# Optimization experiments

Hardware: AMD Instinct MI355X
Metric: run time of the kernel (lower is better)

The kernel has to match this reference:

```python
import jax, jax.numpy as jnp
import numpy as np
from jax import lax

B, C, H, W = 32, 3, 128, 128
NUM_CLASSES = 101
H2, W2 = H // 2, W // 2
N = H2 * W2                      # 4096 graph nodes


def _grid_graph(h, w):
    """4-neighbor bidirectional grid graph + self loops, with GCN sym-norm coeffs."""
    idx = np.arange(h * w).reshape(h, w)
    src = np.concatenate([idx[:, :-1].ravel(), idx[:, 1:].ravel(),
                          idx[:-1, :].ravel(), idx[1:, :].ravel()])
    dst = np.concatenate([idx[:, 1:].ravel(), idx[:, :-1].ravel(),
                          idx[1:, :].ravel(), idx[:-1, :].ravel()])
    # GCNConv default: add self loops, then D^{-1/2} (A+I) D^{-1/2}
    loop = np.arange(h * w)
    src = np.concatenate([src, loop])
    dst = np.concatenate([dst, loop])
    deg = np.bincount(dst, minlength=h * w).astype(np.float32)
    dinv = 1.0 / np.sqrt(deg)
    norm = dinv[src] * dinv[dst]
    return src.astype(np.int32), dst.astype(np.int32), norm.astype(np.float32)


def setup_inputs() -> dict:
    key = jax.random.key(0)
    ks = jax.random.split(key, 9)
    x = jax.random.normal(ks[0], (B, C, H, W), dtype=jnp.float32)
    conv_w = jax.random.normal(ks[1], (32, C, 3, 3), dtype=jnp.float32) * 0.1
    conv_b = jax.random.normal(ks[2], (32,), dtype=jnp.float32) * 0.01
    gcn_w = jax.random.normal(ks[3], (32, 64), dtype=jnp.float32) * 0.15
    gcn_b = jax.random.normal(ks[4], (64,), dtype=jnp.float32) * 0.01
    fc1_w = jax.random.normal(ks[5], (128, 64 * N), dtype=jnp.float32) * (1.0 / 512.0)
    fc1_b = jax.random.normal(ks[6], (128,), dtype=jnp.float32) * 0.01
    fc2_w = jax.random.normal(ks[7], (NUM_CLASSES, 128), dtype=jnp.float32) * 0.08
    fc2_b = jax.random.normal(ks[8], (NUM_CLASSES,), dtype=jnp.float32) * 0.01
    return {"x": x, "conv_w": conv_w, "conv_b": conv_b, "gcn_w": gcn_w,
            "gcn_b": gcn_b, "fc1_w": fc1_w, "fc1_b": fc1_b,
            "fc2_w": fc2_w, "fc2_b": fc2_b}


def reference(x, conv_w, conv_b, gcn_w, gcn_b, fc1_w, fc1_b, fc2_w, fc2_b):
    # conv1 (3x3, pad=1) + relu + maxpool 2x2
    y = lax.conv_general_dilated(x, conv_w, (1, 1), "SAME",
                                 dimension_numbers=("NCHW", "OIHW", "NCHW"))
    y = jax.nn.relu(y + conv_b[None, :, None, None])
    y = lax.reduce_window(y, -jnp.inf, lax.max, (1, 1, 2, 2), (1, 1, 2, 2), "VALID")
    b, c, h2, w2 = y.shape  # [B, 32, 64, 64]

    # faithful torch x.view(B, -1, 32): raw row-major reinterpretation (NOT transpose)
    xg = y.reshape(b, -1, c)  # [B, N, 32]

    # GCNConv(32 -> 64): linear, then gather -> normalize -> scatter-add
    hfeat = jnp.einsum("bnf,fo->bno", xg, gcn_w)  # [B, N, 64]
    src, dst, norm = _grid_graph(h2, w2)
    src = jnp.asarray(src); dst = jnp.asarray(dst)
    coeff = jnp.asarray(norm, hfeat.dtype)[None, :, None]
    msgs = hfeat[:, src, :] * coeff                      # edge-wise gather
    agg = jnp.zeros_like(hfeat).at[:, dst, :].add(msgs)  # scatter-add
    g = jax.nn.relu(agg + gcn_b)

    # flatten + FCs
    flat = g.reshape(b, -1)  # [B, 64*N]
    f1 = jax.nn.relu(flat @ fc1_w.T + fc1_b)
    return f1 @ fc2_w.T + fc2_b
```

## Files before the change

kernel.cpp:

```cpp
#include <hip/hip_runtime.h>


#define K_FC 262144

__global__ __launch_bounds__(256) void k_conv_pool(
    const float* __restrict__ x, const float* __restrict__ cw,
    const float* __restrict__ cb, float* __restrict__ y)
{
    __shared__ float wl[864];
    __shared__ float tin[3 * 34 * 36];

    int blk = blockIdx.x;
    int b = blk >> 4;
    int tile = blk & 15;
    int ph0 = (tile >> 2) << 4;
    int pw0 = (tile & 3) << 4;
    int t = threadIdx.x;

    for (int i = t; i < 864; i += 256) wl[i] = cw[i];

    int r0 = ph0 * 2 - 1;
    int c0 = pw0 * 2 - 1;
    for (int i = t; i < 3 * 34 * 34; i += 256) {
        int ci = i / 1156;
        int rem = i - ci * 1156;
        int yy = rem / 34;
        int xx = rem - yy * 34;
        int gr = r0 + yy, gc = c0 + xx;
        float v = 0.f;
        if (gr >= 0 && gr < 128 && gc >= 0 && gc < 128)
            v = x[((b * 3 + ci) * 128 + gr) * 128 + gc];
        tin[ci * 1224 + yy * 36 + xx] = v;
    }
    __syncthreads();

    int ph = t >> 4, pw = t & 15;
    float p[3][4][4];
#pragma unroll
    for (int ci = 0; ci < 3; ++ci)
#pragma unroll
        for (int dy = 0; dy < 4; ++dy) {
            const float2* row = (const float2*)&tin[ci * 1224 + (2 * ph + dy) * 36 + 2 * pw];
            float2 v0 = row[0], v1 = row[1];
            p[ci][dy][0] = v0.x; p[ci][dy][1] = v0.y;
            p[ci][dy][2] = v1.x; p[ci][dy][3] = v1.y;
        }

    int obase = (b * 32 * 64 + (ph0 + ph)) * 64 + pw0 + pw;
    for (int co = 0; co < 32; ++co) {
        float s00 = 0.f, s01 = 0.f, s10 = 0.f, s11 = 0.f;
#pragma unroll
        for (int ci = 0; ci < 3; ++ci)
#pragma unroll
            for (int ky = 0; ky < 3; ++ky)
#pragma unroll
                for (int kx = 0; kx < 3; ++kx) {
                    float wv = wl[co * 27 + ci * 9 + ky * 3 + kx];
                    s00 = fmaf(p[ci][ky][kx],         wv, s00);
                    s01 = fmaf(p[ci][ky][kx + 1],     wv, s01);
                    s10 = fmaf(p[ci][ky + 1][kx],     wv, s10);
                    s11 = fmaf(p[ci][ky + 1][kx + 1], wv, s11);
                }
        float m = fmaxf(fmaxf(s00, s01), fmaxf(s10, s11)) + cb[co];
        y[obase + co * 4096] = fmaxf(m, 0.f);
    }
}

__device__ __forceinline__ float dinvf(int h, int w) {
    int d = 1 + (w > 0) + (w < 63) + (h > 0) + (h < 63);
    return rsqrtf((float)d);
}

__device__ __forceinline__ void acc4(const float* __restrict__ yb, int hq, int wq,
                                     int fh, float c,
                                     float4& a0, float4& a1, float4& a2, float4& a3)
{
    const float4* s = (const float4*)(yb + (((hq << 6) + wq) << 5) + fh);
    float4 v0 = s[0], v1 = s[1], v2 = s[2], v3 = s[3];
    a0.x = fmaf(c, v0.x, a0.x); a0.y = fmaf(c, v0.y, a0.y);
    a0.z = fmaf(c, v0.z, a0.z); a0.w = fmaf(c, v0.w, a0.w);
    a1.x = fmaf(c, v1.x, a1.x); a1.y = fmaf(c, v1.y, a1.y);
    a1.z = fmaf(c, v1.z, a1.z); a1.w = fmaf(c, v1.w, a1.w);
    a2.x = fmaf(c, v2.x, a2.x); a2.y = fmaf(c, v2.y, a2.y);
    a2.z = fmaf(c, v2.z, a2.z); a2.w = fmaf(c, v2.w, a2.w);
    a3.x = fmaf(c, v3.x, a3.x); a3.y = fmaf(c, v3.y, a3.y);
    a3.z = fmaf(c, v3.z, a3.z); a3.w = fmaf(c, v3.w, a3.w);
}

__global__ __launch_bounds__(256) void k_gcn(
    const float* __restrict__ y, const float* __restrict__ gw,
    const float* __restrict__ gb, float* __restrict__ g)
{
    __shared__ float zl[128 * 36];

    int blk = blockIdx.x;
    int b = blk >> 5;
    int r = blk & 31;
    int t = threadIdx.x;
    const float* yb = y + b * 131072;

    int lane = t & 63;
    int wave = t >> 6;
    float wreg[32];
#pragma unroll
    for (int f = 0; f < 32; ++f) wreg[f] = gw[f * 64 + lane];
    float bias = gb[lane];

    {
        int l = t >> 1;
        int fh = (t & 1) << 4;
        int h = 2 * r + (l >> 6);
        int w = l & 63;
        float dp = dinvf(h, w);
        float4 a0 = {0,0,0,0}, a1 = {0,0,0,0}, a2 = {0,0,0,0}, a3 = {0,0,0,0};
        acc4(yb, h, w, fh, dp * dp, a0, a1, a2, a3);
        if (w > 0)  acc4(yb, h, w - 1, fh, dp * dinvf(h, w - 1), a0, a1, a2, a3);
        if (w < 63) acc4(yb, h, w + 1, fh, dp * dinvf(h, w + 1), a0, a1, a2, a3);
        if (h > 0)  acc4(yb, h - 1, w, fh, dp * dinvf(h - 1, w), a0, a1, a2, a3);
        if (h < 63) acc4(yb, h + 1, w, fh, dp * dinvf(h + 1, w), a0, a1, a2, a3);
        float4* zrow = (float4*)&zl[l * 36 + fh];
        zrow[0] = a0; zrow[1] = a1; zrow[2] = a2; zrow[3] = a3;
    }
    __syncthreads();

    int l0 = wave << 5;
    int pbase = r * 128;
    float* gout = g + (size_t)b * 262144;
    for (int n = 0; n < 32; ++n) {
        int l = l0 + n;
        const float4* zz = (const float4*)&zl[l * 36];
        float acc = bias;
#pragma unroll
        for (int f4 = 0; f4 < 8; ++f4) {
            float4 zv = zz[f4];
            acc = fmaf(zv.x, wreg[f4 * 4 + 0], acc);
            acc = fmaf(zv.y, wreg[f4 * 4 + 1], acc);
            acc = fmaf(zv.z, wreg[f4 * 4 + 2], acc);
            acc = fmaf(zv.w, wreg[f4 * 4 + 3], acc);
        }
        gout[(pbase + l) * 64 + lane] = fmaxf(acc, 0.f);
    }
}

__global__ __launch_bounds__(256, 4) void k_fc1(
    const float* __restrict__ flat, const float* __restrict__ w,
    float* __restrict__ partial)
{
    __shared__ float Wl[128 * 36];
    __shared__ float Al[32 * 36];

    int t = threadIdx.x;
    int blk = blockIdx.x;
    int k0 = blk << 8;

    int sub = t >> 7;
    int tt = t & 127;
    int bg = tt >> 4;
    int b0 = bg << 2;
    int jg = tt & 15;

    float acc[4][8];
#pragma unroll
    for (int i = 0; i < 4; ++i)
#pragma unroll
        for (int jj = 0; jj < 8; ++jj) acc[i][jj] = 0.f;

    for (int s = 0; s < 8; ++s) {
        int ks = k0 + (s << 5);
#pragma unroll
        for (int it = 0; it < 4; ++it) {
            int i = t + (it << 8);
            int j = i >> 3, kq = i & 7;
            float4 v = *(const float4*)(w + (size_t)j * K_FC + ks + (kq << 2));
            *(float4*)&Wl[j * 36 + (kq << 2)] = v;
        }
        {
            int b = t >> 3, kq = t & 7;
            float4 v = *(const float4*)(flat + (size_t)b * K_FC + ks + (kq << 2));
            *(float4*)&Al[b * 36 + (kq << 2)] = v;
        }
        __syncthreads();

#pragma unroll
        for (int c = 0; c < 4; ++c) {
            int kk = (sub << 4) + (c << 2);
            float4 av[4];
#pragma unroll
            for (int i = 0; i < 4; ++i)
                av[i] = *(const float4*)&Al[(b0 + i) * 36 + kk];
#pragma unroll
            for (int jj = 0; jj < 8; ++jj) {
                float4 wv = *(const float4*)&Wl[(jg + (jj << 4)) * 36 + kk];
#pragma unroll
                for (int i = 0; i < 4; ++i) {
                    acc[i][jj] = fmaf(av[i].x, wv.x, acc[i][jj]);
                    acc[i][jj] = fmaf(av[i].y, wv.y, acc[i][jj]);
                    acc[i][jj] = fmaf(av[i].z, wv.z, acc[i][jj]);
                    acc[i][jj] = fmaf(av[i].w, wv.w, acc[i][jj]);
                }
            }
        }
        __syncthreads();
    }

    if (sub == 1) {
#pragma unroll
        for (int i = 0; i < 4; ++i)
#pragma unroll
            for (int jj = 0; jj < 8; ++jj)
                Wl[((i << 3) + jj) * 128 + tt] = acc[i][jj];
    }
    __syncthreads();
    if (sub == 0) {
        float* pout = partial + ((size_t)blk << 12);
#pragma unroll
        for (int i = 0; i < 4; ++i)
#pragma unroll
            for (int jj = 0; jj < 8; ++jj)
                pout[(b0 + i) * 128 + jg + (jj << 4)] =
                    acc[i][jj] + Wl[((i << 3) + jj) * 128 + tt];
    }
}

__global__ __launch_bounds__(256) void k_red(
    const float* __restrict__ partial, float* __restrict__ f1)
{
    __shared__ float4 Sl[256];
    int t = threadIdx.x;
    int e4 = (blockIdx.x << 2) + (t & 3);
    int ng = t >> 2;
    const float4* p = (const float4*)partial;
    float4 a = {0.f, 0.f, 0.f, 0.f};
#pragma unroll
    for (int i = 0; i < 16; ++i) {
        int ns = ng + (i << 6);
        float4 v = p[(size_t)ns * 1024 + e4];
        a.x += v.x; a.y += v.y; a.z += v.z; a.w += v.w;
    }
    Sl[t] = a;
    __syncthreads();
    for (int off = 128; off >= 4; off >>= 1) {
        if (t < off) {
            float4 u = Sl[t], v = Sl[t + off];
            u.x += v.x; u.y += v.y; u.z += v.z; u.w += v.w;
            Sl[t] = u;
        }
        __syncthreads();
    }
    if (t < 4) ((float4*)f1)[(blockIdx.x << 2) + t] = Sl[t];
}

__global__ __launch_bounds__(256) void k_fc2(
    const float* __restrict__ f1, const float* __restrict__ b1,
    const float* __restrict__ w2, const float* __restrict__ b2,
    float* __restrict__ out)
{
    int idx = blockIdx.x * 256 + threadIdx.x;
    if (idx >= 32 * 101) return;
    int b = idx / 101;
    int c = idx - b * 101;
    const float4* fp = (const float4*)(f1 + b * 128);
    const float4* bp = (const float4*)b1;
    const float4* wp = (const float4*)(w2 + c * 128);
    float acc = b2[c];
#pragma unroll
    for (int q = 0; q < 32; ++q) {
        float4 f = fp[q], bb = bp[q], ww = wp[q];
        acc = fmaf(fmaxf(f.x + bb.x, 0.f), ww.x, acc);
        acc = fmaf(fmaxf(f.y + bb.y, 0.f), ww.y, acc);
        acc = fmaf(fmaxf(f.z + bb.z, 0.f), ww.z, acc);
        acc = fmaf(fmaxf(f.w + bb.w, 0.f), ww.w, acc);
    }
    out[idx] = acc;
}

extern "C" void kernel_launch(void* const* d_in, const int* in_sizes, int n_in,
                              void* d_out, int out_size, void* d_ws, size_t ws_size,
                              hipStream_t stream)
{
    const float* x  = (const float*)d_in[0];
    const float* cw = (const float*)d_in[1];
    const float* cb = (const float*)d_in[2];
    const float* gw = (const float*)d_in[3];
    const float* gb = (const float*)d_in[4];
    const float* w1 = (const float*)d_in[5];
    const float* b1 = (const float*)d_in[6];
    const float* w2 = (const float*)d_in[7];
    const float* b2 = (const float*)d_in[8];
    float* out = (float*)d_out;

    float* y       = (float*)d_ws;
    float* g       = y + 4194304;
    float* partial = g + 8388608;
    float* f1      = partial + 4194304;

    k_conv_pool<<<512, 256, 0, stream>>>(x, cw, cb, y);
    k_gcn<<<1024, 256, 0, stream>>>(y, gw, gb, g);
    k_fc1<<<1024, 256, 0, stream>>>(g, w1, partial);
    k_red<<<256, 256, 0, stream>>>(partial, f1);
    k_fc2<<<13, 256, 0, stream>>>(f1, b1, w2, b2, out);
}
```

Before: 281.3 us.

## Restructure GCN linear as register-tiled GEMM and stream fc1 weights directly

The GCN transform now stages aggregated features transposed in shared memory along with the weights and bias, and computes a 4x8 register tile per thread instead of a per-lane dot loop with 32 weight registers. The fc1 split-K kernel stops staging weight tiles in shared memory. It loads the whole 256-wide activation slab once, then each thread streams float4 weight chunks for two output rows straight from global memory, accumulates all 32 batch rows, and reduces across a 4-lane group with shuffles. This targets the fc1 weight traffic, which dominates runtime, by cutting the per-step syncs and LDS round trips. In exchange it uses 64 accumulators per thread, lowering occupancy (launch bounds changed to 3 blocks per CU).

```diff
diff --git a/kernel.cpp b/kernel.cpp
--- a/kernel.cpp
+++ b/kernel.cpp
@@ -91,7 +91,9 @@
     const float* __restrict__ y, const float* __restrict__ gw,
     const float* __restrict__ gb, float* __restrict__ g)
 {
-    __shared__ float zl[128 * 36];
+    __shared__ float zl[32 * 132];
+    __shared__ float wl[32 * 64];
+    __shared__ float bl[64];
 
     int blk = blockIdx.x;
     int b = blk >> 5;
@@ -99,126 +101,138 @@
     int t = threadIdx.x;
     const float* yb = y + b * 131072;
 
-    int lane = t & 63;
-    int wave = t >> 6;
-    float wreg[32];
-#pragma unroll
-    for (int f = 0; f < 32; ++f) wreg[f] = gw[f * 64 + lane];
-    float bias = gb[lane];
+    for (int i = t; i < 512; i += 256) ((float4*)wl)[i] = ((const float4*)gw)[i];
+    if (t < 64) bl[t] = gb[t];
 
     {
         int l = t >> 1;
         int fh = (t & 1) << 4;
         int h = 2 * r + (l >> 6);
-        int w = l & 63;
-        float dp = dinvf(h, w);
+        int wq = l & 63;
+        float dp = dinvf(h, wq);
         float4 a0 = {0,0,0,0}, a1 = {0,0,0,0}, a2 = {0,0,0,0}, a3 = {0,0,0,0};
-        acc4(yb, h, w, fh, dp * dp, a0, a1, a2, a3);
-        if (w > 0)  acc4(yb, h, w - 1, fh, dp * dinvf(h, w - 1), a0, a1, a2, a3);
-        if (w < 63) acc4(yb, h, w + 1, fh, dp * dinvf(h, w + 1), a0, a1, a2, a3);
-        if (h > 0)  acc4(yb, h - 1, w, fh, dp * dinvf(h - 1, w), a0, a1, a2, a3);
-        if (h < 63) acc4(yb, h + 1, w, fh, dp * dinvf(h + 1, w), a0, a1, a2, a3);
-        float4* zrow = (float4*)&zl[l * 36 + fh];
-        zrow[0] = a0; zrow[1] = a1; zrow[2] = a2; zrow[3] = a3;
+        acc4(yb, h, wq, fh, dp * dp, a0, a1, a2, a3);
+        if (wq > 0)  acc4(yb, h, wq - 1, fh, dp * dinvf(h, wq - 1), a0, a1, a2, a3);
+        if (wq < 63) acc4(yb, h, wq + 1, fh, dp * dinvf(h, wq + 1), a0, a1, a2, a3);
+        if (h > 0)   acc4(yb, h - 1, wq, fh, dp * dinvf(h - 1, wq), a0, a1, a2, a3);
+        if (h < 63)  acc4(yb, h + 1, wq, fh, dp * dinvf(h + 1, wq), a0, a1, a2, a3);
+        zl[(fh + 0)  * 132 + l] = a0.x; zl[(fh + 1)  * 132 + l] = a0.y;
+        zl[(fh + 2)  * 132 + l] = a0.z; zl[(fh + 3)  * 132 + l] = a0.w;
+        zl[(fh + 4)  * 132 + l] = a1.x; zl[(fh + 5)  * 132 + l] = a1.y;
+        zl[(fh + 6)  * 132 + l] = a1.z; zl[(fh + 7)  * 132 + l] = a1.w;
+        zl[(fh + 8)  * 132 + l] = a2.x; zl[(fh + 9)  * 132 + l] = a2.y;
+        zl[(fh + 10) * 132 + l] = a2.z; zl[(fh + 11) * 132 + l] = a2.w;
+        zl[(fh + 12) * 132 + l] = a3.x; zl[(fh + 13) * 132 + l] = a3.y;
+        zl[(fh + 14) * 132 + l] = a3.z; zl[(fh + 15) * 132 + l] = a3.w;
     }
     __syncthreads();
 
-    int l0 = wave << 5;
+    int fg = t & 7;
+    int ng = t >> 3;
+    int n0 = ng << 2;
+    int f0 = fg << 3;
+
+    float acc[4][8];
+#pragma unroll
+    for (int i = 0; i < 4; ++i)
+#pragma unroll
+        for (int jj = 0; jj < 8; ++jj) acc[i][jj] = 0.f;
+
+#pragma unroll 8
+    for (int k = 0; k < 32; ++k) {
+        float4 zv  = *(const float4*)&zl[k * 132 + n0];
+        float4 wv0 = *(const float4*)&wl[(k << 6) + f0];
+        float4 wv1 = *(const float4*)&wl[(k << 6) + f0 + 4];
+        float zs[4] = {zv.x, zv.y, zv.z, zv.w};
+        float ws[8] = {wv0.x, wv0.y, wv0.z, wv0.w, wv1.x, wv1.y, wv1.z, wv1.w};
+#pragma unroll
+        for (int i = 0; i < 4; ++i)
+#pragma unroll
+            for (int jj = 0; jj < 8; ++jj)
+                acc[i][jj] = fmaf(zs[i], ws[jj], acc[i][jj]);
+    }
+
     int pbase = r * 128;
     float* gout = g + (size_t)b * 262144;
-    for (int n = 0; n < 32; ++n) {
-        int l = l0 + n;
-        const float4* zz = (const float4*)&zl[l * 36];
-        float acc = bias;
-#pragma unroll
-        for (int f4 = 0; f4 < 8; ++f4) {
-            float4 zv = zz[f4];
-            acc = fmaf(zv.x, wreg[f4 * 4 + 0], acc);
-            acc = fmaf(zv.y, wreg[f4 * 4 + 1], acc);
-            acc = fmaf(zv.z, wreg[f4 * 4 + 2], acc);
-            acc = fmaf(zv.w, wreg[f4 * 4 + 3], acc);
-        }
-        gout[(pbase + l) * 64 + lane] = fmaxf(acc, 0.f);
-    }
-}
-
-__global__ __launch_bounds__(256, 4) void k_fc1(
+#pragma unroll
+    for (int i = 0; i < 4; ++i) {
+        float4 o0, o1;
+        o0.x = fmaxf(acc[i][0] + bl[f0 + 0], 0.f);
+        o0.y = fmaxf(acc[i][1] + bl[f0 + 1], 0.f);
+        o0.z = fmaxf(acc[i][2] + bl[f0 + 2], 0.f);
+        o0.w = fmaxf(acc[i][3] + bl[f0 + 3], 0.f);
+        o1.x = fmaxf(acc[i][4] + bl[f0 + 4], 0.f);
+        o1.y = fmaxf(acc[i][5] + bl[f0 + 5], 0.f);
+        o1.z = fmaxf(acc[i][6] + bl[f0 + 6], 0.f);
+        o1.w = fmaxf(acc[i][7] + bl[f0 + 7], 0.f);
+        float* op = gout + (size_t)(pbase + n0 + i) * 64 + f0;
+        *(float4*)op = o0;
+        *(float4*)(op + 4) = o1;
+    }
+}
+
+__global__ __launch_bounds__(256, 3) void k_fc1(
     const float* __restrict__ flat, const float* __restrict__ w,
     float* __restrict__ partial)
 {
-    __shared__ float Wl[128 * 36];
-    __shared__ float Al[32 * 36];
+    __shared__ float Al[32 * 264];
 
     int t = threadIdx.x;
     int blk = blockIdx.x;
     int k0 = blk << 8;
 
-    int sub = t >> 7;
-    int tt = t & 127;
-    int bg = tt >> 4;
-    int b0 = bg << 2;
-    int jg = tt & 15;
-
-    float acc[4][8];
-#pragma unroll
-    for (int i = 0; i < 4; ++i)
-#pragma unroll
-        for (int jj = 0; jj < 8; ++jj) acc[i][jj] = 0.f;
-
-    for (int s = 0; s < 8; ++s) {
-        int ks = k0 + (s << 5);
-#pragma unroll
-        for (int it = 0; it < 4; ++it) {
-            int i = t + (it << 8);
-            int j = i >> 3, kq = i & 7;
-            float4 v = *(const float4*)(w + (size_t)j * K_FC + ks + (kq << 2));
-            *(float4*)&Wl[j * 36 + (kq << 2)] = v;
+#pragma unroll
+    for (int rr = 0; rr < 8; ++rr) {
+        int idx = (rr << 8) + t;
+        int b = idx >> 6;
+        int c4 = (idx & 63) << 2;
+        *(float4*)&Al[b * 264 + c4] =
+            *(const float4*)(flat + (size_t)b * K_FC + k0 + c4);
+    }
+    __syncthreads();
+
+    int s = t & 3;
+    int j2 = t >> 2;
+    const float* wr0 = w + (size_t)j2 * K_FC + k0 + (s << 2);
+    const float* wr1 = wr0 + (size_t)64 * K_FC;
+
+    float acc0[32], acc1[32];
+#pragma unroll
+    for (int b = 0; b < 32; ++b) { acc0[b] = 0.f; acc1[b] = 0.f; }
+
+#pragma unroll 2
+    for (int q = 0; q < 16; ++q) {
+        float4 wa = *(const float4*)(wr0 + (q << 4));
+        float4 wb = *(const float4*)(wr1 + (q << 4));
+        int kk = (q << 4) + (s << 2);
+#pragma unroll
+        for (int b = 0; b < 32; ++b) {
+            float4 a = *(const float4*)&Al[b * 264 + kk];
+            acc0[b] = fmaf(a.x, wa.x, acc0[b]);
+            acc0[b] = fmaf(a.y, wa.y, acc0[b]);
+            acc0[b] = fmaf(a.z, wa.z, acc0[b]);
+            acc0[b] = fmaf(a.w, wa.w, acc0[b]);
+            acc1[b] = fmaf(a.x, wb.x, acc1[b]);
+            acc1[b] = fmaf(a.y, wb.y, acc1[b]);
+            acc1[b] = fmaf(a.z, wb.z, acc1[b]);
+            acc1[b] = fmaf(a.w, wb.w, acc1[b]);
         }
-        {
-            int b = t >> 3, kq = t & 7;
-            float4 v = *(const float4*)(flat + (size_t)b * K_FC + ks + (kq << 2));
-            *(float4*)&Al[b * 36 + (kq << 2)] = v;
-        }
-        __syncthreads();
-
-#pragma unroll
-        for (int c = 0; c < 4; ++c) {
-            int kk = (sub << 4) + (c << 2);
-            float4 av[4];
-#pragma unroll
-            for (int i = 0; i < 4; ++i)
-                av[i] = *(const float4*)&Al[(b0 + i) * 36 + kk];
-#pragma unroll
-            for (int jj = 0; jj < 8; ++jj) {
-                float4 wv = *(const float4*)&Wl[(jg + (jj << 4)) * 36 + kk];
-#pragma unroll
-                for (int i = 0; i < 4; ++i) {
-                    acc[i][jj] = fmaf(av[i].x, wv.x, acc[i][jj]);
-                    acc[i][jj] = fmaf(av[i].y, wv.y, acc[i][jj]);
-                    acc[i][jj] = fmaf(av[i].z, wv.z, acc[i][jj]);
-                    acc[i][jj] = fmaf(av[i].w, wv.w, acc[i][jj]);
-                }
-            }
-        }
-        __syncthreads();
-    }
-
-    if (sub == 1) {
-#pragma unroll
-        for (int i = 0; i < 4; ++i)
-#pragma unroll
-            for (int jj = 0; jj < 8; ++jj)
-                Wl[((i << 3) + jj) * 128 + tt] = acc[i][jj];
-    }
-    __syncthreads();
-    if (sub == 0) {
-        float* pout = partial + ((size_t)blk << 12);
-#pragma unroll
-        for (int i = 0; i < 4; ++i)
-#pragma unroll
-            for (int jj = 0; jj < 8; ++jj)
-                pout[(b0 + i) * 128 + jg + (jj << 4)] =
-                    acc[i][jj] + Wl[((i << 3) + jj) * 128 + tt];
+    }
+
+#pragma unroll
+    for (int b = 0; b < 32; ++b) {
+        acc0[b] += __shfl_xor(acc0[b], 1);
+        acc0[b] += __shfl_xor(acc0[b], 2);
+        acc1[b] += __shfl_xor(acc1[b], 1);
+        acc1[b] += __shfl_xor(acc1[b], 2);
+    }
+
+    float* pout = partial + ((size_t)blk << 12);
+#pragma unroll
+    for (int i = 0; i < 8; ++i) {
+        int b = (s << 3) + i;
+        pout[b * 128 + j2]      = acc0[b];
+        pout[b * 128 + j2 + 64] = acc1[b];
     }
 }
 
```

Result: no change. 282.8 us (+0.5%).
